# Optimization experiments

Hardware: AMD Instinct MI355X
Metric: run time of the kernel (lower is better)

Reference implementation:

```python
import jax, jax.numpy as jnp
import numpy as np

D = 2048      # hidden
H = 16        # heads
HD = 128      # head dim
E = 64        # experts
K = 8         # top-k
F = 1024      # expert intermediate
B, S = 1, 256
EPS = 1e-05
THETA = 10000.0
SCALE = 0.08838834764831845  # 1/sqrt(128)


def _rms(x, w):
    return x * jax.lax.rsqrt(jnp.mean(x * x, axis=-1, keepdims=True) + EPS) * w


def _rotate_half(x):
    h = x.shape[-1] // 2
    return jnp.concatenate([-x[..., h:], x[..., :h]], axis=-1)


def setup_inputs() -> dict:
    key = jax.random.key(0)
    ks = jax.random.split(key, 16)
    std = 0.02
    return {
        "x": jax.random.normal(ks[0], (B, S, D), jnp.float32),
        "ln1_w": jnp.ones((D,), jnp.float32),
        "q_w": jax.random.normal(ks[1], (D, D), jnp.float32) * std,
        "k_w": jax.random.normal(ks[2], (D, D), jnp.float32) * std,
        "v_w": jax.random.normal(ks[3], (D, D), jnp.float32) * std,
        "o_w": jax.random.normal(ks[4], (D, D), jnp.float32) * std,
        "qn_w": jnp.ones((D,), jnp.float32),
        "kn_w": jnp.ones((D,), jnp.float32),
        "ln2_w": jnp.ones((D,), jnp.float32),
        "router_w": jax.random.normal(ks[5], (E, D), jnp.float32) * std,
        "gate_w": jax.random.normal(ks[6], (E, F, D), jnp.float32) * std,
        "up_w": jax.random.normal(ks[7], (E, F, D), jnp.float32) * std,
        "down_w": jax.random.normal(ks[8], (E, D, F), jnp.float32) * std,
    }


def reference(x, ln1_w, q_w, k_w, v_w, o_w, qn_w, kn_w, ln2_w,
              router_w, gate_w, up_w, down_w):
    b, s, d = x.shape
    # ---- attention ----
    xn = _rms(x, ln1_w)
    q = _rms(jnp.einsum('bsd,od->bso', xn, q_w), qn_w)
    k = _rms(jnp.einsum('bsd,od->bso', xn, k_w), kn_w)
    v = jnp.einsum('bsd,od->bso', xn, v_w)
    q = q.reshape(b, s, H, HD).transpose(0, 2, 1, 3)  # [b,h,s,hd]
    k = k.reshape(b, s, H, HD).transpose(0, 2, 1, 3)
    v = v.reshape(b, s, H, HD).transpose(0, 2, 1, 3)
    # RoPE
    inv_freq = 1.0 / (THETA ** (jnp.arange(0, HD, 2, dtype=jnp.float32) / HD))
    ang = jnp.arange(s, dtype=jnp.float32)[:, None] * inv_freq[None, :]  # [s, hd/2]
    emb = jnp.concatenate([ang, ang], axis=-1)
    cos, sin = jnp.cos(emb).astype(x.dtype), jnp.sin(emb).astype(x.dtype)
    q = q * cos + _rotate_half(q) * sin
    k = k * cos + _rotate_half(k) * sin
    scores = jnp.einsum('bhqd,bhkd->bhqk', q, k) * SCALE
    causal = jnp.tril(jnp.ones((s, s), bool))
    scores = jnp.where(causal, scores, jnp.finfo(scores.dtype).min)
    attn = jax.nn.softmax(scores, axis=-1)
    ctx = jnp.einsum('bhqk,bhkd->bhqd', attn, v)
    ctx = ctx.transpose(0, 2, 1, 3).reshape(b, s, d)
    h = x + jnp.einsum('bsd,od->bso', ctx, o_w)
    # ---- MoE ----
    hn = _rms(h, ln2_w)
    logits = jnp.einsum('bsd,ed->bse', hn, router_w)
    probs = jax.nn.softmax(logits.astype(jnp.float32), axis=-1)
    vals, idx = jax.lax.top_k(probs, K)  # [b,s,K]
    # dense combine weights [b,s,E]; OLMoE does not renormalize top-k probs
    combine = jnp.sum(jax.nn.one_hot(idx, E, dtype=jnp.float32) * vals[..., None], axis=-2)
    combine = combine.reshape(-1, E).astype(x.dtype)  # [T,E]
    xf = hn.reshape(-1, d)                            # [T,D]
    g = jnp.einsum('td,efd->etf', xf, gate_w)         # [E,T,F]
    u = jnp.einsum('td,efd->etf', xf, up_w)
    mid = jax.nn.silu(g) * u
    eo = jnp.einsum('etf,edf->etd', mid, down_w)      # [E,T,D]
    y = jnp.einsum('te,etd->td', combine, eo).reshape(b, s, d)
    return h + y
```

## Files before the change

kernel.cpp:

```cpp
#include <hip/hip_runtime.h>
#include <math.h>

#define DHID 2048
#define TOK 256
#define NHEAD 16
#define HDIM 128
#define NEXP 64
#define KSEL 8
#define FFD 1024
#define RMSEPS 1e-5f
#define ATTNSCALE 0.08838834764831845f

typedef short bf16x8 __attribute__((ext_vector_type(8)));
typedef float f32x4 __attribute__((ext_vector_type(4)));

__device__ __forceinline__ float bf2f(unsigned short u){
  union { unsigned int u; float f; } c; c.u = ((unsigned int)u)<<16; return c.f;
}
__device__ __forceinline__ unsigned short f2bf(float f){
  union { float f; unsigned int u; } c; c.f = f;
  unsigned int u = c.u + 0x7fffu + ((c.u>>16)&1u);
  return (unsigned short)(u>>16);
}
__device__ __forceinline__ unsigned int pk2(float a, float b){
  return (unsigned int)f2bf(a) | ((unsigned int)f2bf(b)<<16);
}
__device__ __forceinline__ bf16x8 pack8f(float4 a, float4 b){
  union { uint4 u; bf16x8 v; } c;
  c.u = make_uint4(pk2(a.x,a.y), pk2(a.z,a.w), pk2(b.x,b.y), pk2(b.z,b.w));
  return c.v;
}
__device__ __forceinline__ bf16x8 as_bf8(uint4 u){
  union { uint4 u; bf16x8 v; } c; c.u = u; return c.v;
}
__device__ __forceinline__ void gl2lds16(const void* g, void* l){
  __builtin_amdgcn_global_load_lds(
    (const __attribute__((address_space(1))) unsigned int*)g,
    (__attribute__((address_space(3))) unsigned int*)l, 16, 0, 0);
}

__global__ __launch_bounds__(256) void rms_kernel(const float* __restrict__ x,
    const float* __restrict__ w, unsigned short* __restrict__ obf,
    float* __restrict__ of32)
{
  int row = blockIdx.x, tid = threadIdx.x;
  const float* xr = x + (size_t)row*DHID;
  float4 a = *(const float4*)(xr + tid*8);
  float4 b = *(const float4*)(xr + tid*8 + 4);
  float ss = a.x*a.x+a.y*a.y+a.z*a.z+a.w*a.w + b.x*b.x+b.y*b.y+b.z*b.z+b.w*b.w;
  #pragma unroll
  for(int o=32;o>0;o>>=1) ss += __shfl_down(ss,o);
  __shared__ float red[4];
  if((tid&63)==0) red[tid>>6]=ss;
  __syncthreads();
  float r = rsqrtf((red[0]+red[1]+red[2]+red[3])*(1.0f/DHID) + RMSEPS);
  float v[8] = {a.x,a.y,a.z,a.w,b.x,b.y,b.z,b.w};
  unsigned short ob[8];
  #pragma unroll
  for(int j=0;j<8;j++){
    float val = v[j]*r*w[tid*8+j];
    ob[j]=f2bf(val);
    if(of32) of32[(size_t)row*DHID + tid*8 + j] = val;
  }
  uint4 o4;
  o4.x = (unsigned int)ob[0] | ((unsigned int)ob[1]<<16);
  o4.y = (unsigned int)ob[2] | ((unsigned int)ob[3]<<16);
  o4.z = (unsigned int)ob[4] | ((unsigned int)ob[5]<<16);
  o4.w = (unsigned int)ob[6] | ((unsigned int)ob[7]<<16);
  *(uint4*)(obf + (size_t)row*DHID + tid*8) = o4;
}

__global__ void rope_table_kernel(float* __restrict__ cs, float* __restrict__ sn){
  int i = blockIdx.x*256 + threadIdx.x;
  int s = i>>6, j = i&63;
  float invf = powf(10000.0f, -(float)j*(1.0f/64.0f));
  float ang = (float)s * invf;
  cs[i] = cosf(ang); sn[i] = sinf(ang);
}

__global__ __launch_bounds__(256) void gemm_qkv_kernel(
    const unsigned short* __restrict__ A,
    const float* __restrict__ qw, const float* __restrict__ kw, const float* __restrict__ vw,
    float* __restrict__ qo, float* __restrict__ ko, float* __restrict__ vo)
{
  int nt = blockIdx.x, mt = blockIdx.y;
  int which = nt>>5, nb = nt&31;
  const float* W = (which==0)? qw : (which==1)? kw : vw;
  float* OUT = (which==0)? qo : (which==1)? ko : vo;
  int n0 = nb*64, m0 = mt*64;
  __shared__ unsigned short As[64*64];
  __shared__ unsigned short Bs[64*64];
  int tid = threadIdx.x;
  int wid = tid>>6, lane = tid&63;
  int wm = wid>>1, wn = wid&1;
  int lr = lane&15, lg = lane>>4;
  int sr = tid>>2, sq = tid&3;
  f32x4 acc[2][2] = {};
  const unsigned short* Ap = A + (size_t)(m0+sr)*DHID + sq*16;
  const float* Bp = W + (size_t)(n0+sr)*DHID + sq*16;
  for(int k0=0;k0<DHID;k0+=64){
    uint4 a0 = *(const uint4*)(Ap + k0);
    uint4 a1 = *(const uint4*)(Ap + k0 + 8);
    float4 b0 = *(const float4*)(Bp + k0);
    float4 b1 = *(const float4*)(Bp + k0 + 4);
    float4 b2 = *(const float4*)(Bp + k0 + 8);
    float4 b3 = *(const float4*)(Bp + k0 + 12);
    int x7 = sr&7;
    *(uint4*)&As[sr*64 + (((sq*2)  ^ x7)*8)] = a0;
    *(uint4*)&As[sr*64 + (((sq*2+1)^ x7)*8)] = a1;
    uint4 p0 = make_uint4(pk2(b0.x,b0.y),pk2(b0.z,b0.w),pk2(b1.x,b1.y),pk2(b1.z,b1.w));
    uint4 p1 = make_uint4(pk2(b2.x,b2.y),pk2(b2.z,b2.w),pk2(b3.x,b3.y),pk2(b3.z,b3.w));
    *(uint4*)&Bs[sr*64 + (((sq*2)  ^ x7)*8)] = p0;
    *(uint4*)&Bs[sr*64 + (((sq*2+1)^ x7)*8)] = p1;
    __syncthreads();
    #pragma unroll
    for(int ki=0;ki<2;ki++){
      bf16x8 af[2], bfr[2];
      #pragma unroll
      for(int mi=0;mi<2;mi++){
        int r = wm*32 + mi*16 + lr;
        af[mi] = *(const bf16x8*)&As[r*64 + (((ki*4+lg)^(r&7))*8)];
      }
      #pragma unroll
      for(int ni=0;ni<2;ni++){
        int r = wn*32 + ni*16 + lr;
        bfr[ni] = *(const bf16x8*)&Bs[r*64 + (((ki*4+lg)^(r&7))*8)];
      }
      #pragma unroll
      for(int mi=0;mi<2;mi++)
        #pragma unroll
        for(int ni=0;ni<2;ni++)
          acc[mi][ni] = __builtin_amdgcn_mfma_f32_16x16x32_bf16(af[mi], bfr[ni], acc[mi][ni], 0,0,0);
    }
    __syncthreads();
  }
  #pragma unroll
  for(int mi=0;mi<2;mi++){
    #pragma unroll
    for(int ni=0;ni<2;ni++){
      int col = n0 + wn*32 + ni*16 + lr;
      int rowb = m0 + wm*32 + mi*16 + lg*4;
      #pragma unroll
      for(int rg=0;rg<4;rg++)
        OUT[(size_t)(rowb+rg)*DHID + col] = acc[mi][ni][rg];
    }
  }
}

__global__ __launch_bounds__(256) void gemm_o_kernel(const float* __restrict__ A,
  const float* __restrict__ W, const float* __restrict__ X,
  float* __restrict__ H, float* __restrict__ O)
{
  int nb = blockIdx.x, mt = blockIdx.y;
  int n0 = nb*64, m0 = mt*64;
  __shared__ unsigned short As[64*64];
  __shared__ unsigned short Bs[64*64];
  int tid = threadIdx.x;
  int wid = tid>>6, lane = tid&63;
  int wm = wid>>1, wn = wid&1;
  int lr = lane&15, lg = lane>>4;
  int sr = tid>>2, sq = tid&3;
  f32x4 acc[2][2] = {};
  const float* Ap = A + (size_t)(m0+sr)*DHID + sq*16;
  const float* Bp = W + (size_t)(n0+sr)*DHID + sq*16;
  for(int k0=0;k0<DHID;k0+=64){
    float4 a0=*(const float4*)(Ap+k0),   a1=*(const float4*)(Ap+k0+4);
    float4 a2=*(const float4*)(Ap+k0+8), a3=*(const float4*)(Ap+k0+12);
    float4 b0=*(const float4*)(Bp+k0),   b1=*(const float4*)(Bp+k0+4);
    float4 b2=*(const float4*)(Bp+k0+8), b3=*(const float4*)(Bp+k0+12);
    int x7 = sr&7;
    uint4 pa0 = make_uint4(pk2(a0.x,a0.y),pk2(a0.z,a0.w),pk2(a1.x,a1.y),pk2(a1.z,a1.w));
    uint4 pa1 = make_uint4(pk2(a2.x,a2.y),pk2(a2.z,a2.w),pk2(a3.x,a3.y),pk2(a3.z,a3.w));
    uint4 pb0 = make_uint4(pk2(b0.x,b0.y),pk2(b0.z,b0.w),pk2(b1.x,b1.y),pk2(b1.z,b1.w));
    uint4 pb1 = make_uint4(pk2(b2.x,b2.y),pk2(b2.z,b2.w),pk2(b3.x,b3.y),pk2(b3.z,b3.w));
    *(uint4*)&As[sr*64 + (((sq*2)  ^ x7)*8)] = pa0;
    *(uint4*)&As[sr*64 + (((sq*2+1)^ x7)*8)] = pa1;
    *(uint4*)&Bs[sr*64 + (((sq*2)  ^ x7)*8)] = pb0;
    *(uint4*)&Bs[sr*64 + (((sq*2+1)^ x7)*8)] = pb1;
    __syncthreads();
    #pragma unroll
    for(int ki=0;ki<2;ki++){
      bf16x8 af[2], bfr[2];
      #pragma unroll
      for(int mi=0;mi<2;mi++){
        int r = wm*32 + mi*16 + lr;
        af[mi] = *(const bf16x8*)&As[r*64 + (((ki*4+lg)^(r&7))*8)];
      }
      #pragma unroll
      for(int ni=0;ni<2;ni++){
        int r = wn*32 + ni*16 + lr;
        bfr[ni] = *(const bf16x8*)&Bs[r*64 + (((ki*4+lg)^(r&7))*8)];
      }
      #pragma unroll
      for(int mi=0;mi<2;mi++)
        #pragma unroll
        for(int ni=0;ni<2;ni++)
          acc[mi][ni] = __builtin_amdgcn_mfma_f32_16x16x32_bf16(af[mi], bfr[ni], acc[mi][ni], 0,0,0);
    }
    __syncthreads();
  }
  #pragma unroll
  for(int mi=0;mi<2;mi++){
    #pragma unroll
    for(int ni=0;ni<2;ni++){
      int col = n0 + wn*32 + ni*16 + lr;
      int rowb = m0 + wm*32 + mi*16 + lg*4;
      #pragma unroll
      for(int rg=0;rg<4;rg++){
        size_t idx = (size_t)(rowb+rg)*DHID + col;
        float v = acc[mi][ni][rg] + X[idx];
        H[idx] = v; O[idx] = v;
      }
    }
  }
}

__global__ __launch_bounds__(256) void qknorm_rope_kernel(const float* __restrict__ in,
   const float* __restrict__ w, const float* __restrict__ cs, const float* __restrict__ sn,
   float* __restrict__ out)
{
  int t = blockIdx.x, tid = threadIdx.x;
  __shared__ float xs[DHID];
  const float* xr = in + (size_t)t*DHID;
  float4 a = *(const float4*)(xr + tid*8);
  float4 b = *(const float4*)(xr + tid*8 + 4);
  *(float4*)&xs[tid*8] = a; *(float4*)&xs[tid*8+4] = b;
  float ss = a.x*a.x+a.y*a.y+a.z*a.z+a.w*a.w + b.x*b.x+b.y*b.y+b.z*b.z+b.w*b.w;
  #pragma unroll
  for(int o=32;o>0;o>>=1) ss += __shfl_down(ss,o);
  __shared__ float red[4];
  if((tid&63)==0) red[tid>>6]=ss;
  __syncthreads();
  float r = rsqrtf((red[0]+red[1]+red[2]+red[3])*(1.0f/DHID) + RMSEPS);
  int hh = tid>>4, jb = (tid&15)*4;
  #pragma unroll
  for(int p=0;p<4;p++){
    int j = jb+p;
    int i0 = hh*HDIM + j, i1 = i0+64;
    float va = xs[i0]*r*w[i0];
    float vb = xs[i1]*r*w[i1];
    float c = cs[t*64+j], s = sn[t*64+j];
    out[((size_t)(hh*TOK + t))*HDIM + j]    = va*c - vb*s;
    out[((size_t)(hh*TOK + t))*HDIM + j+64] = vb*c + va*s;
  }
}

__global__ __launch_bounds__(256) void vreshape_kernel(const float* __restrict__ v,
    float* __restrict__ vh)
{
  int t = blockIdx.x, tid = threadIdx.x;
  int i = tid*8;
  int hh = i>>7, d0 = i&127;
  float4 a = *(const float4*)(v + (size_t)t*DHID + i);
  float4 b = *(const float4*)(v + (size_t)t*DHID + i + 4);
  *(float4*)(vh + ((size_t)(hh*TOK+t))*HDIM + d0)     = a;
  *(float4*)(vh + ((size_t)(hh*TOK+t))*HDIM + d0 + 4) = b;
}

__global__ __launch_bounds__(256) void attn_kernel(const float* __restrict__ qh,
  const float* __restrict__ kh, const float* __restrict__ vh, float* __restrict__ ctx)
{
  int head = blockIdx.x>>4, qt = blockIdx.x&15;
  __shared__ float qs[16][132];
  __shared__ float sc[16][260];
  __shared__ float red[16][16];
  __shared__ float rmx[16], rsm[16];
  int tid = threadIdx.x;
  {
    int r = tid>>4, c = (tid&15)*8;
    const float* src = qh + ((size_t)(head*TOK + qt*16 + r))*HDIM + c;
    *(float4*)&qs[r][c]   = *(const float4*)(src);
    *(float4*)&qs[r][c+4] = *(const float4*)(src+4);
  }
  __syncthreads();
  int qi = tid&15, kk = tid>>4;
  int qg = qt*16 + qi;
  for(int k=kk; k<=qg; k+=16){
    const float* kp = kh + ((size_t)(head*TOK + k))*HDIM;
    float d = 0.f;
    #pragma unroll 8
    for(int c=0;c<128;c+=4){
      float4 kv = *(const float4*)(kp + c);
      float4 qv = *(const float4*)&qs[qi][c];
      d += qv.x*kv.x + qv.y*kv.y + qv.z*kv.z + qv.w*kv.w;
    }
    sc[qi][k] = d*ATTNSCALE;
  }
  float m = -1e30f;
  for(int k=kk;k<=qg;k+=16) m = fmaxf(m, sc[qi][k]);
  red[qi][kk] = m;
  __syncthreads();
  if(kk==0){
    float mm=-1e30f;
    #pragma unroll
    for(int j=0;j<16;j++) mm = fmaxf(mm, red[qi][j]);
    rmx[qi]=mm;
  }
  __syncthreads();
  float mm = rmx[qi];
  float s = 0.f;
  for(int k=kk;k<=qg;k+=16){ float pp = expf(sc[qi][k]-mm); sc[qi][k]=pp; s+=pp; }
  red[qi][kk]=s;
  __syncthreads();
  if(kk==0){
    float t_=0.f;
    #pragma unroll
    for(int j=0;j<16;j++) t_ += red[qi][j];
    rsm[qi]=t_;
  }
  __syncthreads();
  int dg = kk;
  float acc[8]={0,0,0,0,0,0,0,0};
  const float* vp = vh + (size_t)head*TOK*HDIM + dg*8;
  for(int k=0;k<=qg;k++){
    float p = sc[qi][k];
    float4 v0 = *(const float4*)(vp + (size_t)k*HDIM);
    float4 v1 = *(const float4*)(vp + (size_t)k*HDIM + 4);
    acc[0]+=p*v0.x; acc[1]+=p*v0.y; acc[2]+=p*v0.z; acc[3]+=p*v0.w;
    acc[4]+=p*v1.x; acc[5]+=p*v1.y; acc[6]+=p*v1.z; acc[7]+=p*v1.w;
  }
  float inv = 1.0f/rsm[qi];
  float* op = ctx + ((size_t)(qt*16+qi))*DHID + head*HDIM + dg*8;
  *(float4*)(op)   = make_float4(acc[0]*inv, acc[1]*inv, acc[2]*inv, acc[3]*inv);
  *(float4*)(op+4) = make_float4(acc[4]*inv, acc[5]*inv, acc[6]*inv, acc[7]*inv);
}

__global__ __launch_bounds__(256) void router_kernel(const float* __restrict__ hn,
    const float* __restrict__ rw, int* __restrict__ counts, int* __restrict__ toklist,
    float* __restrict__ wlist)
{
  int t = blockIdx.x, tid = threadIdx.x;
  __shared__ float xs[DHID];
  __shared__ float part[NEXP*4];
  __shared__ float probs[NEXP];
  *(float4*)&xs[tid*8]   = *(const float4*)(hn + (size_t)t*DHID + tid*8);
  *(float4*)&xs[tid*8+4] = *(const float4*)(hn + (size_t)t*DHID + tid*8+4);
  __syncthreads();
  int e = tid&63, c = tid>>6;
  const float* w = rw + (size_t)e*DHID + c*512;
  const float* xc = xs + c*512;
  float d = 0.f;
  for(int i=0;i<512;i+=4){
    float4 wv = *(const float4*)(w+i);
    d += xc[i]*wv.x + xc[i+1]*wv.y + xc[i+2]*wv.z + xc[i+3]*wv.w;
  }
  part[c*64 + e] = d;
  __syncthreads();
  if(tid<64){
    float logit = part[tid] + part[64+tid] + part[128+tid] + part[192+tid];
    float m = logit;
    #pragma unroll
    for(int o=32;o>0;o>>=1) m = fmaxf(m, __shfl_xor(m,o));
    float p = expf(logit - m);
    float s = p;
    #pragma unroll
    for(int o=32;o>0;o>>=1) s += __shfl_xor(s,o);
    probs[tid] = p/s;
  }
  __syncthreads();
  if(tid==0){
    unsigned long long used = 0ull;
    for(int r=0;r<KSEL;r++){
      float best = -1.f; int bi = 0;
      for(int j=0;j<NEXP;j++){
        if(!((used>>j)&1ull) && probs[j]>best){ best=probs[j]; bi=j; }
      }
      used |= (1ull<<bi);
      int slot = atomicAdd(&counts[bi],1);
      toklist[bi*TOK+slot] = t;
      wlist[bi*TOK+slot] = best;
    }
  }
}

__global__ void scan_kernel(const int* __restrict__ counts, int* __restrict__ offs){
  int e = threadIdx.x;
  int c = counts[e];
  int v = c;
  #pragma unroll
  for(int o=1;o<64;o<<=1){
    int n = __shfl_up(v,o);
    if(e>=o) v += n;
  }
  offs[e] = v - c;
}

__global__ __launch_bounds__(256) void moe_gateup_kernel(const unsigned short* __restrict__ hnb,
  const float* __restrict__ gw, const float* __restrict__ uw,
  const int* __restrict__ counts, const int* __restrict__ offs,
  const int* __restrict__ toklist, const float* __restrict__ wlist,
  unsigned short* __restrict__ mid)
{
  int fb = blockIdx.x, e = blockIdx.y, mc = blockIdx.z;
  int cnt = counts[e];
  if(mc*32 >= cnt) return;
  int base = offs[e];
  __shared__ float Bg[2*64*64];
  __shared__ float Bu[2*64*64];
  int tid = threadIdx.x;
  int w = tid>>6, lane = tid&63;
  int wm = w>>1, wn = w&1, lr = lane&15, lg = lane>>4;

  int l15 = lane&15, l4 = lane>>4;
  const float* gsrc[4]; const float* usrc[4]; int ldst[4];
  #pragma unroll
  for(int i=0;i<4;i++){
    int r0 = w*16 + i*4;
    int r  = r0 + l4;
    int srccol = (l15 ^ (r&15)) << 2;
    size_t grow = (size_t)(e*FFD + fb*64 + r)*DHID + srccol;
    gsrc[i] = gw + grow;
    usrc[i] = uw + grow;
    ldst[i] = r0*64;
  }
  int aslot = mc*32 + wm*16 + lr;
  int acl = (aslot<cnt)? aslot : (cnt-1);
  int atok = toklist[e*TOK + acl];
  const unsigned short* Ap = hnb + (size_t)atok*DHID + lg*8;

  f32x4 ag[2]={}, au[2]={};

  #define STAGE_GU(b,k0) { \
    _Pragma("unroll") \
    for(int i=0;i<4;i++){ \
      gl2lds16(gsrc[i]+(k0), &Bg[(b)*4096 + ldst[i]]); \
      gl2lds16(usrc[i]+(k0), &Bu[(b)*4096 + ldst[i]]); \
    } }

  STAGE_GU(0,0)
  uint4 a0 = *(const uint4*)(Ap);
  uint4 a1 = *(const uint4*)(Ap + 32);
  __syncthreads();

  int buf = 0;
  const int NT = DHID/64;
  for(int t=0;t<NT;t++){
    int k0 = t*64;
    if(t+1<NT) STAGE_GU(buf^1, k0+64)
    uint4 n0=a0, n1=a1;
    if(t+1<NT){ n0 = *(const uint4*)(Ap + k0 + 64); n1 = *(const uint4*)(Ap + k0 + 96); }
    bf16x8 af[2] = { as_bf8(a0), as_bf8(a1) };
    bf16x8 gf[2][2], uf[2][2];
    #pragma unroll
    for(int ni=0;ni<2;ni++){
      int R = wn*32 + ni*16 + lr;
      #pragma unroll
      for(int ki=0;ki<2;ki++){
        int u  = ((ki*4+lg)<<1) ^ lr;
        int o1 = buf*4096 + R*64 + (u<<2);
        int o2 = o1 ^ 4;
        float4 g0 = *(const float4*)&Bg[o1];
        float4 g1 = *(const float4*)&Bg[o2];
        float4 u0 = *(const float4*)&Bu[o1];
        float4 u1 = *(const float4*)&Bu[o2];
        gf[ni][ki] = pack8f(g0,g1);
        uf[ni][ki] = pack8f(u0,u1);
      }
    }
    #pragma unroll
    for(int ki=0;ki<2;ki++){
      #pragma unroll
      for(int ni=0;ni<2;ni++){
        ag[ni] = __builtin_amdgcn_mfma_f32_16x16x32_bf16(af[ki], gf[ni][ki], ag[ni], 0,0,0);
        au[ni] = __builtin_amdgcn_mfma_f32_16x16x32_bf16(af[ki], uf[ni][ki], au[ni], 0,0,0);
      }
    }
    __syncthreads();
    buf ^= 1; a0 = n0; a1 = n1;
  }
  #undef STAGE_GU

  #pragma unroll
  for(int ni=0;ni<2;ni++){
    int f = fb*64 + wn*32 + ni*16 + lr;
    #pragma unroll
    for(int rg=0;rg<4;rg++){
      int sl = wm*16 + lg*4 + rg;
      int slot = mc*32 + sl;
      if(slot < cnt){
        float cw = wlist[e*TOK + slot];
        float g = ag[ni][rg], u = au[ni][rg];
        float mval = g/(1.0f+expf(-g))*u*cw;
        mid[((size_t)(base+slot))*FFD + f] = f2bf(mval);
      }
    }
  }
}

__global__ __launch_bounds__(256) void moe_down_kernel(const unsigned short* __restrict__ mid,
  const float* __restrict__ dwn, const int* __restrict__ counts, const int* __restrict__ offs,
  const int* __restrict__ toklist, float* __restrict__ out)
{
  int nb=blockIdx.x, e=blockIdx.y, mc=blockIdx.z;
  int cnt=counts[e];
  if(mc*32>=cnt) return;
  int base=offs[e];
  __shared__ float Bd[2*64*64];
  int tid=threadIdx.x;
  int w=tid>>6, lane=tid&63, wm=w>>1, wn=w&1, lr=lane&15, lg=lane>>4;

  int l15 = lane&15, l4 = lane>>4;
  const float* dsrc[4]; int ldst[4];
  #pragma unroll
  for(int i=0;i<4;i++){
    int r0 = w*16 + i*4;
    int r  = r0 + l4;
    int srccol = (l15 ^ (r&15)) << 2;
    dsrc[i] = dwn + (size_t)(e*DHID + nb*64 + r)*FFD + srccol;
    ldst[i] = r0*64;
  }
  int slot0 = mc*32 + wm*16 + lr;
  int sla = (slot0<cnt)? slot0 : (cnt-1);
  const unsigned short* Ap = mid + (size_t)(base+sla)*FFD + lg*8;
  int mytok[4];
  #pragma unroll
  for(int rg=0;rg<4;rg++){
    int sl = mc*32 + wm*16 + lg*4 + rg;
    mytok[rg] = toklist[e*TOK + ((sl<cnt)? sl : (cnt-1))];
  }

  f32x4 acc[2]={};

  #define STAGE_D(b,k0) { \
    _Pragma("unroll") \
    for(int i=0;i<4;i++) gl2lds16(dsrc[i]+(k0), &Bd[(b)*4096 + ldst[i]]); }

  STAGE_D(0,0)
  uint4 a0 = *(const uint4*)(Ap);
  uint4 a1 = *(const uint4*)(Ap + 32);
  __syncthreads();

  int buf = 0;
  const int NT = FFD/64;
  for(int t=0;t<NT;t++){
    int k0 = t*64;
    if(t+1<NT) STAGE_D(buf^1, k0+64)
    uint4 n0=a0, n1=a1;
    if(t+1<NT){ n0 = *(const uint4*)(Ap + k0 + 64); n1 = *(const uint4*)(Ap + k0 + 96); }
    bf16x8 af[2] = { as_bf8(a0), as_bf8(a1) };
    bf16x8 df[2][2];
    #pragma unroll
    for(int ni=0;ni<2;ni++){
      int R = wn*32 + ni*16 + lr;
      #pragma unroll
      for(int ki=0;ki<2;ki++){
        int u  = ((ki*4+lg)<<1) ^ lr;
        int o1 = buf*4096 + R*64 + (u<<2);
        int o2 = o1 ^ 4;
        float4 d0 = *(const float4*)&Bd[o1];
        float4 d1 = *(const float4*)&Bd[o2];
        df[ni][ki] = pack8f(d0,d1);
      }
    }
    #pragma unroll
    for(int ki=0;ki<2;ki++){
      #pragma unroll
      for(int ni=0;ni<2;ni++)
        acc[ni] = __builtin_amdgcn_mfma_f32_16x16x32_bf16(af[ki], df[ni][ki], acc[ni], 0,0,0);
    }
    __syncthreads();
    buf ^= 1; a0 = n0; a1 = n1;
  }
  #undef STAGE_D

  #pragma unroll
  for(int ni=0;ni<2;ni++){
    int d = nb*64 + wn*32 + ni*16 + lr;
    #pragma unroll
    for(int rg=0;rg<4;rg++){
      int sl=wm*16+lg*4+rg, slot=mc*32+sl;
      if(slot<cnt) atomicAdd(out + (size_t)mytok[rg]*DHID + d, acc[ni][rg]);
    }
  }
}

extern "C" void kernel_launch(void* const* d_in, const int* in_sizes, int n_in,
                              void* d_out, int out_size, void* d_ws, size_t ws_size,
                              hipStream_t stream)
{
  (void)in_sizes; (void)n_in; (void)out_size; (void)ws_size;
  const float* x    = (const float*)d_in[0];
  const float* ln1w = (const float*)d_in[1];
  const float* qw   = (const float*)d_in[2];
  const float* kw   = (const float*)d_in[3];
  const float* vw   = (const float*)d_in[4];
  const float* ow   = (const float*)d_in[5];
  const float* qnw  = (const float*)d_in[6];
  const float* knw  = (const float*)d_in[7];
  const float* ln2w = (const float*)d_in[8];
  const float* rw   = (const float*)d_in[9];
  const float* gw   = (const float*)d_in[10];
  const float* uw   = (const float*)d_in[11];
  const float* dwn  = (const float*)d_in[12];
  float* out = (float*)d_out;

  char* p = (char*)d_ws;
  auto alloc = [&](size_t bytes)->void*{ void* r = (void*)p; p += (bytes + 255) & ~(size_t)255; return r; };
  unsigned short* xnb = (unsigned short*)alloc((size_t)TOK*DHID*2);
  float* qf   = (float*)alloc((size_t)TOK*DHID*4);
  float* kf   = (float*)alloc((size_t)TOK*DHID*4);
  float* vf   = (float*)alloc((size_t)TOK*DHID*4);
  float* qh   = (float*)alloc((size_t)TOK*DHID*4);
  float* kh   = (float*)alloc((size_t)TOK*DHID*4);
  float* vh   = (float*)alloc((size_t)TOK*DHID*4);
  float* ctx  = (float*)alloc((size_t)TOK*DHID*4);
  float* hbuf = (float*)alloc((size_t)TOK*DHID*4);
  float* hnf  = (float*)alloc((size_t)TOK*DHID*4);
  unsigned short* hnb = (unsigned short*)alloc((size_t)TOK*DHID*2);
  float* csb  = (float*)alloc((size_t)TOK*64*4);
  float* snb  = (float*)alloc((size_t)TOK*64*4);
  int* counts = (int*)alloc(NEXP*4);
  int* offs   = (int*)alloc(NEXP*4);
  int* toklist= (int*)alloc((size_t)NEXP*TOK*4);
  float* wlist= (float*)alloc((size_t)NEXP*TOK*4);
  unsigned short* mid = (unsigned short*)alloc((size_t)TOK*KSEL*FFD*2);

  rope_table_kernel<<<64,256,0,stream>>>(csb,snb);
  rms_kernel<<<TOK,256,0,stream>>>(x, ln1w, xnb, nullptr);
  gemm_qkv_kernel<<<dim3(96,4),256,0,stream>>>(xnb,qw,kw,vw,qf,kf,vf);
  qknorm_rope_kernel<<<TOK,256,0,stream>>>(qf,qnw,csb,snb,qh);
  qknorm_rope_kernel<<<TOK,256,0,stream>>>(kf,knw,csb,snb,kh);
  vreshape_kernel<<<TOK,256,0,stream>>>(vf,vh);
  attn_kernel<<<256,256,0,stream>>>(qh,kh,vh,ctx);
  gemm_o_kernel<<<dim3(32,4),256,0,stream>>>(ctx,ow,x,hbuf,out);
  rms_kernel<<<TOK,256,0,stream>>>(hbuf, ln2w, hnb, hnf);
  hipMemsetAsync(counts,0,NEXP*4,stream);
  router_kernel<<<TOK,256,0,stream>>>(hnf,rw,counts,toklist,wlist);
  scan_kernel<<<1,64,0,stream>>>(counts,offs);
  moe_gateup_kernel<<<dim3(16,NEXP,8),256,0,stream>>>(hnb,gw,uw,counts,offs,toklist,wlist,mid);
  moe_down_kernel<<<dim3(32,NEXP,8),256,0,stream>>>(mid,dwn,counts,offs,toklist,out);
}
```

Baseline: 695.9 us.

## Use explicit vmcnt waits and split barriers for double-buffered MoE GEMM pipelines

Restructures the gate/up and down expert GEMM loops into a manually unrolled two-stage pipeline. Both buffers are prefetched up front, and each stage waits with s_waitcnt vmcnt on only its own loads instead of draining everything at __syncthreads. This keeps the next tile's global-to-LDS loads in flight during compute. Token-index loads in the down kernel move to the epilogue to cut register pressure during the main loop. The hand-counted vmcnt values must match the number of outstanding loads exactly, or the kernel can read stale LDS data.

```diff
diff --git a/kernel.cpp b/kernel.cpp
--- a/kernel.cpp
+++ b/kernel.cpp
@@ -38,6 +38,9 @@
     (const __attribute__((address_space(1))) unsigned int*)g,
     (__attribute__((address_space(3))) unsigned int*)l, 16, 0, 0);
 }
+
+#define WAITV(N) { asm volatile("s_waitcnt vmcnt(" #N ")" ::: "memory"); __builtin_amdgcn_sched_barrier(0); }
+#define WAITL0   { asm volatile("s_waitcnt lgkmcnt(0)" ::: "memory"); __builtin_amdgcn_sched_barrier(0); }
 
 __global__ __launch_bounds__(256) void rms_kernel(const float* __restrict__ x,
     const float* __restrict__ w, unsigned short* __restrict__ obf,
@@ -420,55 +423,63 @@
 
   f32x4 ag[2]={}, au[2]={};
 
-  #define STAGE_GU(b,k0) { \
+  #define STAGE_GU(bofs,k0) { \
     _Pragma("unroll") \
     for(int i=0;i<4;i++){ \
-      gl2lds16(gsrc[i]+(k0), &Bg[(b)*4096 + ldst[i]]); \
-      gl2lds16(usrc[i]+(k0), &Bu[(b)*4096 + ldst[i]]); \
+      gl2lds16(gsrc[i]+(k0), &Bg[(bofs) + ldst[i]]); \
+      gl2lds16(usrc[i]+(k0), &Bu[(bofs) + ldst[i]]); \
     } }
 
-  STAGE_GU(0,0)
-  uint4 a0 = *(const uint4*)(Ap);
-  uint4 a1 = *(const uint4*)(Ap + 32);
-  __syncthreads();
-
-  int buf = 0;
+  #define COMPUTE_GU(bofs,aa0,aa1) { \
+    bf16x8 af0 = as_bf8(aa0), af1 = as_bf8(aa1); \
+    _Pragma("unroll") \
+    for(int ni=0;ni<2;ni++){ \
+      int R = wn*32 + ni*16 + lr; \
+      _Pragma("unroll") \
+      for(int ki=0;ki<2;ki++){ \
+        int u  = ((ki*4+lg)<<1) ^ lr; \
+        int o1 = (bofs) + R*64 + (u<<2); \
+        int o2 = o1 ^ 4; \
+        bf16x8 gfr = pack8f(*(const float4*)&Bg[o1], *(const float4*)&Bg[o2]); \
+        bf16x8 ufr = pack8f(*(const float4*)&Bu[o1], *(const float4*)&Bu[o2]); \
+        bf16x8 afk = ki ? af1 : af0; \
+        ag[ni] = __builtin_amdgcn_mfma_f32_16x16x32_bf16(afk, gfr, ag[ni], 0,0,0); \
+        au[ni] = __builtin_amdgcn_mfma_f32_16x16x32_bf16(afk, ufr, au[ni], 0,0,0); \
+      } \
+    } }
+
   const int NT = DHID/64;
-  for(int t=0;t<NT;t++){
-    int k0 = t*64;
-    if(t+1<NT) STAGE_GU(buf^1, k0+64)
-    uint4 n0=a0, n1=a1;
-    if(t+1<NT){ n0 = *(const uint4*)(Ap + k0 + 64); n1 = *(const uint4*)(Ap + k0 + 96); }
-    bf16x8 af[2] = { as_bf8(a0), as_bf8(a1) };
-    bf16x8 gf[2][2], uf[2][2];
-    #pragma unroll
-    for(int ni=0;ni<2;ni++){
-      int R = wn*32 + ni*16 + lr;
-      #pragma unroll
-      for(int ki=0;ki<2;ki++){
-        int u  = ((ki*4+lg)<<1) ^ lr;
-        int o1 = buf*4096 + R*64 + (u<<2);
-        int o2 = o1 ^ 4;
-        float4 g0 = *(const float4*)&Bg[o1];
-        float4 g1 = *(const float4*)&Bg[o2];
-        float4 u0 = *(const float4*)&Bu[o1];
-        float4 u1 = *(const float4*)&Bu[o2];
-        gf[ni][ki] = pack8f(g0,g1);
-        uf[ni][ki] = pack8f(u0,u1);
-      }
-    }
-    #pragma unroll
-    for(int ki=0;ki<2;ki++){
-      #pragma unroll
-      for(int ni=0;ni<2;ni++){
-        ag[ni] = __builtin_amdgcn_mfma_f32_16x16x32_bf16(af[ki], gf[ni][ki], ag[ni], 0,0,0);
-        au[ni] = __builtin_amdgcn_mfma_f32_16x16x32_bf16(af[ki], uf[ni][ki], au[ni], 0,0,0);
-      }
-    }
-    __syncthreads();
-    buf ^= 1; a0 = n0; a1 = n1;
+  STAGE_GU(0, 0)
+  uint4 aA0 = *(const uint4*)(Ap);
+  uint4 aA1 = *(const uint4*)(Ap + 32);
+  STAGE_GU(4096, 64)
+  uint4 aB0 = *(const uint4*)(Ap + 64);
+  uint4 aB1 = *(const uint4*)(Ap + 96);
+
+  for(int tt=0; tt<NT; tt+=2){
+    WAITV(10)
+    __builtin_amdgcn_s_barrier();
+    COMPUTE_GU(0, aA0, aA1)
+    WAITL0
+    __builtin_amdgcn_s_barrier();
+    if(tt+2<NT){
+      STAGE_GU(0, (tt+2)*64)
+      aA0 = *(const uint4*)(Ap + (tt+2)*64);
+      aA1 = *(const uint4*)(Ap + (tt+2)*64 + 32);
+    }
+    if(tt+3<NT){ WAITV(10) } else { WAITV(0) }
+    __builtin_amdgcn_s_barrier();
+    COMPUTE_GU(4096, aB0, aB1)
+    WAITL0
+    __builtin_amdgcn_s_barrier();
+    if(tt+3<NT){
+      STAGE_GU(4096, (tt+3)*64)
+      aB0 = *(const uint4*)(Ap + (tt+3)*64);
+      aB1 = *(const uint4*)(Ap + (tt+3)*64 + 32);
+    }
   }
   #undef STAGE_GU
+  #undef COMPUTE_GU
 
   #pragma unroll
   for(int ni=0;ni<2;ni++){
@@ -512,56 +523,61 @@
   int slot0 = mc*32 + wm*16 + lr;
   int sla = (slot0<cnt)? slot0 : (cnt-1);
   const unsigned short* Ap = mid + (size_t)(base+sla)*FFD + lg*8;
-  int mytok[4];
-  #pragma unroll
-  for(int rg=0;rg<4;rg++){
-    int sl = mc*32 + wm*16 + lg*4 + rg;
-    mytok[rg] = toklist[e*TOK + ((sl<cnt)? sl : (cnt-1))];
-  }
 
   f32x4 acc[2]={};
 
-  #define STAGE_D(b,k0) { \
+  #define STAGE_D(bofs,k0) { \
     _Pragma("unroll") \
-    for(int i=0;i<4;i++) gl2lds16(dsrc[i]+(k0), &Bd[(b)*4096 + ldst[i]]); }
-
-  STAGE_D(0,0)
-  uint4 a0 = *(const uint4*)(Ap);
-  uint4 a1 = *(const uint4*)(Ap + 32);
-  __syncthreads();
-
-  int buf = 0;
+    for(int i=0;i<4;i++) gl2lds16(dsrc[i]+(k0), &Bd[(bofs) + ldst[i]]); }
+
+  #define COMPUTE_D(bofs,aa0,aa1) { \
+    bf16x8 af0 = as_bf8(aa0), af1 = as_bf8(aa1); \
+    _Pragma("unroll") \
+    for(int ni=0;ni<2;ni++){ \
+      int R = wn*32 + ni*16 + lr; \
+      _Pragma("unroll") \
+      for(int ki=0;ki<2;ki++){ \
+        int u  = ((ki*4+lg)<<1) ^ lr; \
+        int o1 = (bofs) + R*64 + (u<<2); \
+        int o2 = o1 ^ 4; \
+        bf16x8 dfr = pack8f(*(const float4*)&Bd[o1], *(const float4*)&Bd[o2]); \
+        bf16x8 afk = ki ? af1 : af0; \
+        acc[ni] = __builtin_amdgcn_mfma_f32_16x16x32_bf16(afk, dfr, acc[ni], 0,0,0); \
+      } \
+    } }
+
   const int NT = FFD/64;
-  for(int t=0;t<NT;t++){
-    int k0 = t*64;
-    if(t+1<NT) STAGE_D(buf^1, k0+64)
-    uint4 n0=a0, n1=a1;
-    if(t+1<NT){ n0 = *(const uint4*)(Ap + k0 + 64); n1 = *(const uint4*)(Ap + k0 + 96); }
-    bf16x8 af[2] = { as_bf8(a0), as_bf8(a1) };
-    bf16x8 df[2][2];
-    #pragma unroll
-    for(int ni=0;ni<2;ni++){
-      int R = wn*32 + ni*16 + lr;
-      #pragma unroll
-      for(int ki=0;ki<2;ki++){
-        int u  = ((ki*4+lg)<<1) ^ lr;
-        int o1 = buf*4096 + R*64 + (u<<2);
-        int o2 = o1 ^ 4;
-        float4 d0 = *(const float4*)&Bd[o1];
-        float4 d1 = *(const float4*)&Bd[o2];
-        df[ni][ki] = pack8f(d0,d1);
-      }
-    }
-    #pragma unroll
-    for(int ki=0;ki<2;ki++){
-      #pragma unroll
-      for(int ni=0;ni<2;ni++)
-        acc[ni] = __builtin_amdgcn_mfma_f32_16x16x32_bf16(af[ki], df[ni][ki], acc[ni], 0,0,0);
-    }
-    __syncthreads();
-    buf ^= 1; a0 = n0; a1 = n1;
+  STAGE_D(0, 0)
+  uint4 aA0 = *(const uint4*)(Ap);
+  uint4 aA1 = *(const uint4*)(Ap + 32);
+  STAGE_D(4096, 64)
+  uint4 aB0 = *(const uint4*)(Ap + 64);
+  uint4 aB1 = *(const uint4*)(Ap + 96);
+
+  for(int tt=0; tt<NT; tt+=2){
+    WAITV(6)
+    __builtin_amdgcn_s_barrier();
+    COMPUTE_D(0, aA0, aA1)
+    WAITL0
+    __builtin_amdgcn_s_barrier();
+    if(tt+2<NT){
+      STAGE_D(0, (tt+2)*64)
+      aA0 = *(const uint4*)(Ap + (tt+2)*64);
+      aA1 = *(const uint4*)(Ap + (tt+2)*64 + 32);
+    }
+    if(tt+3<NT){ WAITV(6) } else { WAITV(0) }
+    __builtin_amdgcn_s_barrier();
+    COMPUTE_D(4096, aB0, aB1)
+    WAITL0
+    __builtin_amdgcn_s_barrier();
+    if(tt+3<NT){
+      STAGE_D(4096, (tt+3)*64)
+      aB0 = *(const uint4*)(Ap + (tt+3)*64);
+      aB1 = *(const uint4*)(Ap + (tt+3)*64 + 32);
+    }
   }
   #undef STAGE_D
+  #undef COMPUTE_D
 
   #pragma unroll
   for(int ni=0;ni<2;ni++){
@@ -569,7 +585,10 @@
     #pragma unroll
     for(int rg=0;rg<4;rg++){
       int sl=wm*16+lg*4+rg, slot=mc*32+sl;
-      if(slot<cnt) atomicAdd(out + (size_t)mytok[rg]*DHID + d, acc[ni][rg]);
+      if(slot<cnt){
+        int tok = toklist[e*TOK + slot];
+        atomicAdd(out + (size_t)tok*DHID + d, acc[ni][rg]);
+      }
     }
   }
 }
```

Measured after the change: 752.9 us. +8.2%, slower.
